# Performance work log

Measured on AMD Instinct MI355X. Metric: run time of the kernel, lower is better.

## Reference

```python
import jax, jax.numpy as jnp
import numpy as np

WS = 7       # window size
SHIFT = 3    # shift size (ws//2)
NH = 16      # num heads
DIM = 512    # channels
HH = 112
WW = 112
HIDDEN = int(DIM * 4.0)
EPS = 1e-5


def _rel_index():
    # Swin relative position index, [N, N] ints into the bias table
    coords = np.stack(np.meshgrid(np.arange(WS), np.arange(WS), indexing='ij')).reshape(2, -1)
    rel = coords[:, :, None] - coords[:, None, :]
    rel = rel.transpose(1, 2, 0) + (WS - 1)
    rel[:, :, 0] *= 2 * WS - 1
    return rel.sum(-1)


def _attn_mask():
    # shifted-window mask on HH x WW (already multiples of WS) -> [nW, N, N] with 0 / -1e9
    img = np.zeros((HH, WW), np.int32)
    cnt = 0
    sl = (slice(0, -WS), slice(-WS, -SHIFT), slice(-SHIFT, None))
    for h in sl:
        for w in sl:
            img[h, w] = cnt
            cnt += 1
    win = img.reshape(HH // WS, WS, WW // WS, WS).transpose(0, 2, 1, 3).reshape(-1, WS * WS)
    diff = win[:, None, :] - win[:, :, None]
    return np.where(diff == 0, 0.0, -1e9).astype(np.float32)


def setup_inputs() -> dict:
    key = jax.random.key(0)
    ks = jax.random.split(key, 8)
    s = 0.02
    return {
        'x': jax.random.normal(ks[0], (DIM, HH, WW), jnp.float32),
        'norm1_w': jnp.ones((DIM,), jnp.float32),
        'norm1_b': jnp.zeros((DIM,), jnp.float32),
        'qkv_w': jax.random.normal(ks[1], (3 * DIM, DIM), jnp.float32) * s,
        'qkv_b': jnp.zeros((3 * DIM,), jnp.float32),
        'proj_w': jax.random.normal(ks[2], (DIM, DIM), jnp.float32) * s,
        'proj_b': jnp.zeros((DIM,), jnp.float32),
        'rpb_table': jax.random.normal(ks[3], ((2 * WS - 1) ** 2, NH), jnp.float32) * s,
        'norm2_w': jnp.ones((DIM,), jnp.float32),
        'norm2_b': jnp.zeros((DIM,), jnp.float32),
        'fc1_w': jax.random.normal(ks[4], (HIDDEN, DIM), jnp.float32) * s,
        'fc1_b': jnp.zeros((HIDDEN,), jnp.float32),
        'fc2_w': jax.random.normal(ks[5], (DIM, HIDDEN), jnp.float32) * s,
        'fc2_b': jnp.zeros((DIM,), jnp.float32),
    }


def _ln(x_hwc, w, b):
    m = x_hwc.mean(-1, keepdims=True)
    v = x_hwc.var(-1, keepdims=True)
    return (x_hwc - m) / jnp.sqrt(v + EPS) * w + b


def reference(x, norm1_w, norm1_b, qkv_w, qkv_b, proj_w, proj_b, rpb_table,
              norm2_w, norm2_b, fc1_w, fc1_b, fc2_w, fc2_b):
    C, H, W = x.shape
    ws = WS
    N = ws * ws
    hd = C // NH
    scale = 1.0 / np.sqrt(hd).astype(np.float32)

    x_hwc = jnp.moveaxis(x, 0, -1)                       # [H,W,C]
    xn = _ln(x_hwc, norm1_w, norm1_b)
    xs = jnp.roll(xn, (-SHIFT, -SHIFT), (0, 1))          # cyclic shift
    # window partition -> [nW, N, C]
    xw = xs.reshape(H // ws, ws, W // ws, ws, C).transpose(0, 2, 1, 3, 4).reshape(-1, N, C)

    qkv = xw @ qkv_w.T + qkv_b                            # [nW,N,3C]
    q, k, v = jnp.split(qkv, 3, -1)
    heads = lambda t: t.reshape(-1, N, NH, hd).transpose(0, 2, 1, 3)  # [nW,H,N,hd]
    q, k, v = heads(q), heads(k), heads(v)

    attn = jnp.einsum('whnd,whmd->whnm', q * scale, k)    # [nW,H,N,N]
    idx = jnp.asarray(_rel_index().reshape(-1))
    bias = rpb_table[idx].reshape(N, N, NH).transpose(2, 0, 1)  # [H,N,N]
    mask = jnp.asarray(_attn_mask())                       # [nW,N,N]
    attn = attn + bias[None] + mask[:, None]
    attn = jax.nn.softmax(attn, -1)

    out = jnp.einsum('whnm,whmd->whnd', attn, v).transpose(0, 2, 1, 3).reshape(-1, N, C)
    out = out @ proj_w.T + proj_b
    # window unpartition + reverse shift
    out = out.reshape(H // ws, W // ws, ws, ws, C).transpose(0, 2, 1, 3, 4).reshape(H, W, C)
    out = jnp.roll(out, (SHIFT, SHIFT), (0, 1))

    x1 = x_hwc + out                                       # residual (DropPath rate 0)
    x2 = _ln(x1, norm2_w, norm2_b)
    h = jax.nn.gelu(x2.reshape(-1, C) @ fc1_w.T + fc1_b)
    m = (h @ fc2_w.T + fc2_b).reshape(H, W, C)
    y = x1 + m
    return jnp.moveaxis(y, -1, 0)                          # back to [C,H,W]
```

## Files before the change

### kernel.cpp

```cpp
#include <hip/hip_runtime.h>

#define NPIX 12544
#define CDIM 512
#define QKVN 1536
#define HIDDEN 2048

typedef unsigned short u16;
typedef unsigned int u32;

typedef short bf16x8 __attribute__((ext_vector_type(8)));
typedef float f32x4 __attribute__((ext_vector_type(4)));

static __device__ __forceinline__ u16 f2bf(float f) {
  u32 u = __float_as_uint(f);
  return (u16)((u + 0x7fffu + ((u >> 16) & 1u)) >> 16);
}
static __device__ __forceinline__ u32 pack2(float a, float b) {
  return (u32)f2bf(a) | ((u32)f2bf(b) << 16);
}
static __device__ __forceinline__ u32 packtrunc2(float lo, float hi) {
  return __builtin_amdgcn_perm(__float_as_uint(hi), __float_as_uint(lo), 0x07060302u);
}
static __device__ __forceinline__ void async_ld16(const void* g, void* l) {
  __builtin_amdgcn_global_load_lds((__attribute__((address_space(1))) void*)g,
                                   (__attribute__((address_space(3))) void*)l, 16, 0, 0);
}

__global__ __launch_bounds__(256) void f32_to_bf16(const float* __restrict__ in, u16* __restrict__ out) {
  const int i = blockIdx.x * 256 + threadIdx.x;
  const float4 v = ((const float4*)in)[i];
  ushort4 u;
  u.x = f2bf(v.x); u.y = f2bf(v.y); u.z = f2bf(v.z); u.w = f2bf(v.w);
  ((ushort4*)out)[i] = u;
}

__global__ __launch_bounds__(256) void ln1_partial(const float* __restrict__ x,
                                                   float* __restrict__ psum, float* __restrict__ pssq) {
  const int p = blockIdx.x * 256 + threadIdx.x;
  const int c0 = blockIdx.y * 32;
  float s = 0.f, ss = 0.f;
#pragma unroll
  for (int c = 0; c < 32; c++) {
    const float v = x[(long)(c0 + c) * NPIX + p];
    s += v; ss += v * v;
  }
  psum[blockIdx.y * NPIX + p] = s;
  pssq[blockIdx.y * NPIX + p] = ss;
}

__global__ __launch_bounds__(256) void ln1_stats(const float* __restrict__ psum, const float* __restrict__ pssq,
                                                 float* __restrict__ mean, float* __restrict__ rstd) {
  const int p = blockIdx.x * 256 + threadIdx.x;
  float s = 0.f, ss = 0.f;
#pragma unroll
  for (int ch = 0; ch < 16; ch++) { s += psum[ch * NPIX + p]; ss += pssq[ch * NPIX + p]; }
  const float m = s * (1.f / 512.f);
  const float v = ss * (1.f / 512.f) - m * m;
  mean[p] = m;
  rstd[p] = rsqrtf(v + 1e-5f);
}

__global__ __launch_bounds__(256) void ln1_shift_part(const float* __restrict__ x,
    const float* __restrict__ mean, const float* __restrict__ rstd,
    const float* __restrict__ gw, const float* __restrict__ gb, u16* __restrict__ xw) {
  __shared__ float tile[32][65];
  const int p0 = blockIdx.x * 64;
  const int c0 = blockIdx.y * 32;
  const int t = threadIdx.x;
  {
    const int pl = t & 63;
    const int cl0 = t >> 6;
#pragma unroll
    for (int r = 0; r < 8; r++) {
      const int cl = r * 4 + cl0;
      tile[cl][pl] = x[(long)(c0 + cl) * NPIX + p0 + pl];
    }
  }
  __syncthreads();
  const int cl = t & 31;
  const int g = t >> 5;
  const float wc = gw[c0 + cl];
  const float bc = gb[c0 + cl];
#pragma unroll
  for (int pass = 0; pass < 8; pass++) {
    const int pl = pass * 8 + g;
    const int p = p0 + pl;
    const int h = p / 112;
    const int w = p - h * 112;
    int hs = h + 109; if (hs >= 112) hs -= 112;
    int ws2 = w + 109; if (ws2 >= 112) ws2 -= 112;
    const int hq = hs / 7, wq = ws2 / 7;
    const int tok = (hq * 16 + wq) * 49 + (hs - hq * 7) * 7 + (ws2 - wq * 7);
    const float val = (tile[cl][pl] - mean[p]) * rstd[p] * wc + bc;
    xw[(long)tok * 512 + c0 + cl] = f2bf(val);
  }
}

template<bool OUT_BF16, bool DO_GELU, bool REMAP>
__global__ __launch_bounds__(256, 2) void gemm_bt(
    const u16* __restrict__ A, const u16* __restrict__ B,
    const float* __restrict__ bias, void* __restrict__ out,
    const int N, const int K) {
  __shared__ __align__(16) u16 Asm[128 * 32];
  __shared__ __align__(16) u16 Bsm[128 * 32];
  const int M0 = blockIdx.x << 7;
  const int N0 = blockIdx.y << 7;
  const int t = threadIdx.x;
  const int wave = t >> 6;
  const int lane = t & 63;
  const int l15 = lane & 15;
  const int quad = lane >> 4;
  const int wm = wave & 1;
  const int wn = wave >> 1;

  f32x4 acc[4][4] = {};

  for (int k0 = 0; k0 < K; k0 += 32) {
#pragma unroll
    for (int i = 0; i < 2; i++) {
      const int flatbase = i * 256 + wave * 64;
      const int FL = flatbase + lane;
      const int row = FL >> 2;
      const int chunk = FL & 3;
      async_ld16(A + (long)(M0 + row) * K + k0 + chunk * 8, &Asm[flatbase * 8]);
      async_ld16(B + (long)(N0 + row) * K + k0 + chunk * 8, &Bsm[flatbase * 8]);
    }
    __syncthreads();
    bf16x8 af[4], bfr[4];
#pragma unroll
    for (int im = 0; im < 4; im++)
      af[im] = *(const bf16x8*)&Asm[(wm * 64 + im * 16 + l15) * 32 + quad * 8];
#pragma unroll
    for (int in = 0; in < 4; in++)
      bfr[in] = *(const bf16x8*)&Bsm[(wn * 64 + in * 16 + l15) * 32 + quad * 8];
#pragma unroll
    for (int im = 0; im < 4; im++)
#pragma unroll
      for (int in = 0; in < 4; in++)
        acc[im][in] = __builtin_amdgcn_mfma_f32_16x16x32_bf16(af[im], bfr[in], acc[im][in], 0, 0, 0);
    __syncthreads();
  }

#pragma unroll
  for (int im = 0; im < 4; im++) {
#pragma unroll
    for (int in = 0; in < 4; in++) {
      const int col = N0 + wn * 64 + in * 16 + l15;
      const float bv = bias[col];
#pragma unroll
      for (int r = 0; r < 4; r++) {
        const int row = M0 + wm * 64 + im * 16 + quad * 4 + r;
        float v = acc[im][in][r] + bv;
        if (DO_GELU) {
          const float z2 = 1.5957691216f * (v + 0.044715f * v * v * v);
          v = v / (1.0f + __expf(-z2));
        }
        long orow = row;
        if (REMAP) {
          const int win = row / 49;
          const int nn = row - win * 49;
          const int nq = nn / 7;
          const int hs = (win >> 4) * 7 + nq;
          const int wsx = (win & 15) * 7 + (nn - nq * 7);
          int h = hs + 3; if (h >= 112) h -= 112;
          int w = wsx + 3; if (w >= 112) w -= 112;
          orow = h * 112 + w;
        }
        if (OUT_BF16) ((u16*)out)[orow * (long)N + col] = f2bf(v);
        else          ((float*)out)[orow * (long)N + col] = v;
      }
    }
  }
}

__global__ __launch_bounds__(256) void build_biasT(const float* __restrict__ rpb, float* __restrict__ biasT) {
  const int cls = blockIdx.x >> 4;
  const int head = blockIdx.x & 15;
  for (int e = threadIdx.x; e < 4096; e += 256) {
    const int j = e >> 6;
    const int i = e & 63;
    float v;
    if (j >= 49) v = -1e9f;
    else if (i >= 49) v = 0.f;
    else {
      const int ri = i / 7, ci = i - (i / 7) * 7;
      const int rj = j / 7, cj = j - (j / 7) * 7;
      v = rpb[((ri - rj + 6) * 13 + (ci - cj + 6)) * 16 + head];
      const int lhi = (cls & 2) ? (ri < 4 ? 1 : 2) : 0;
      const int lwi = (cls & 1) ? (ci < 4 ? 1 : 2) : 0;
      const int lhj = (cls & 2) ? (rj < 4 ? 1 : 2) : 0;
      const int lwj = (cls & 1) ? (cj < 4 ? 1 : 2) : 0;
      if (lhi * 3 + lwi != lhj * 3 + lwj) v = -1e9f;
    }
    biasT[(long)blockIdx.x * 4096 + e] = v;
  }
}

__global__ __launch_bounds__(256, 3) void attn_mfma(
    const u16* __restrict__ qkv, const float* __restrict__ biasT, u16* __restrict__ out) {
  __shared__ __align__(16) u16 slds[24576];
  const int t = threadIdx.x;
  const int wave = t >> 6;
  const int lane = t & 63;
  const int l15 = lane & 15;
  const int quad = lane >> 4;
  const int win = blockIdx.x >> 2;
  const int head = (blockIdx.x & 3) * 4 + wave;
  const int cls = (((win >> 4) == 15) ? 2 : 0) | (((win & 15) == 15) ? 1 : 0);

  u16* Qb  = slds + wave * 6144;
  u16* Kb  = Qb + 2048;
  u16* Vtb = Qb + 4096;
  u16* Pb  = Qb;

  const int rrow = lane >> 2;
  const int chunk = lane & 3;
  uint4 vv[4];
#pragma unroll
  for (int it = 0; it < 4; it++) {
    const int row = it * 16 + rrow;
    const int jc = row < 49 ? row : 48;
    const long gbase = (long)(win * 49 + jc) * 1536 + head * 32 + chunk * 8;
    async_ld16(qkv + gbase,       Qb + it * 512 + lane * 8);
    async_ld16(qkv + gbase + 512, Kb + it * 512 + lane * 8);
    vv[it] = *(const uint4*)(qkv + gbase + 1024);
  }
  __syncthreads();

#pragma unroll
  for (int it = 0; it < 4; it++) {
    const int row = it * 16 + rrow;
    const u32* w = (const u32*)&vv[it];
#pragma unroll
    for (int tt = 0; tt < 8; tt++) {
      const int d = chunk * 8 + tt;
      const u16 val = (tt & 1) ? (u16)(w[tt >> 1] >> 16) : (u16)(w[tt >> 1] & 0xffffu);
      Vtb[d * 64 + (row ^ (((d >> 2) & 3) << 4))] = val;
    }
  }

  bf16x8 kfrag[4], qfrag[4];
#pragma unroll
  for (int jm = 0; jm < 4; jm++)
    kfrag[jm] = *(const bf16x8*)(Kb + (jm * 16 + l15) * 32 + quad * 8);
#pragma unroll
  for (int in = 0; in < 4; in++)
    qfrag[in] = *(const bf16x8*)(Qb + (in * 16 + l15) * 32 + quad * 8);
  f32x4 sacc[4][4] = {};
#pragma unroll
  for (int jm = 0; jm < 4; jm++)
#pragma unroll
    for (int in = 0; in < 4; in++)
      sacc[jm][in] = __builtin_amdgcn_mfma_f32_16x16x32_bf16(kfrag[jm], qfrag[in], sacc[jm][in], 0, 0, 0);

  const float* bT = biasT + (long)(cls * 16 + head) * 4096;
  const float sc = 0.17677669529663687f;
#pragma unroll
  for (int jm = 0; jm < 4; jm++) {
    const float* bp = bT + (jm * 16 + quad * 4) * 64 + l15;
#pragma unroll
    for (int in = 0; in < 4; in++)
#pragma unroll
      for (int r = 0; r < 4; r++)
        sacc[jm][in][r] = sacc[jm][in][r] * sc + bp[r * 64 + in * 16];
  }
  float linv[4];
#pragma unroll
  for (int in = 0; in < 4; in++) {
    float m = -1e30f;
#pragma unroll
    for (int jm = 0; jm < 4; jm++)
#pragma unroll
      for (int r = 0; r < 4; r++) m = fmaxf(m, sacc[jm][in][r]);
    m = fmaxf(m, __shfl_xor(m, 16));
    m = fmaxf(m, __shfl_xor(m, 32));
    float s = 0.f;
#pragma unroll
    for (int jm = 0; jm < 4; jm++)
#pragma unroll
      for (int r = 0; r < 4; r++) {
        const float e = __expf(sacc[jm][in][r] - m);
        sacc[jm][in][r] = e; s += e;
      }
    s += __shfl_xor(s, 16);
    s += __shfl_xor(s, 32);
    linv[in] = __builtin_amdgcn_rcpf(s);
  }

#pragma unroll
  for (int in = 0; in < 4; in++) {
    const int i = in * 16 + l15;
    const int rot = (l15 & 3) << 4;
#pragma unroll
    for (int jm = 0; jm < 4; jm++) {
      const u32 lo = packtrunc2(sacc[jm][in][0], sacc[jm][in][1]);
      const u32 hi = packtrunc2(sacc[jm][in][2], sacc[jm][in][3]);
      uint2 u; u.x = lo; u.y = hi;
      *(uint2*)(Pb + i * 64 + ((jm * 16 + quad * 4) ^ rot)) = u;
    }
  }

  f32x4 oacc[2][4] = {};
#pragma unroll
  for (int ks = 0; ks < 2; ks++) {
    bf16x8 vtf[2], pf[4];
#pragma unroll
    for (int dm = 0; dm < 2; dm++)
      vtf[dm] = *(const bf16x8*)(Vtb + (dm * 16 + l15) * 64 + ((ks * 32 + quad * 8) ^ ((l15 >> 2) << 4)));
#pragma unroll
    for (int in = 0; in < 4; in++)
      pf[in] = *(const bf16x8*)(Pb + (in * 16 + l15) * 64 + ((ks * 32 + quad * 8) ^ ((l15 & 3) << 4)));
#pragma unroll
    for (int dm = 0; dm < 2; dm++)
#pragma unroll
      for (int in = 0; in < 4; in++)
        oacc[dm][in] = __builtin_amdgcn_mfma_f32_16x16x32_bf16(vtf[dm], pf[in], oacc[dm][in], 0, 0, 0);
  }

#pragma unroll
  for (int in = 0; in < 4; in++) {
    const int i = in * 16 + l15;
    if (i < 49) {
      const float inv = linv[in];
      const long base = (long)(win * 49 + i) * 512 + head * 32 + quad * 4;
#pragma unroll
      for (int dm = 0; dm < 2; dm++) {
        const float v0 = oacc[dm][in][0] * inv, v1 = oacc[dm][in][1] * inv;
        const float v2 = oacc[dm][in][2] * inv, v3 = oacc[dm][in][3] * inv;
        uint2 u; u.x = packtrunc2(v0, v1); u.y = packtrunc2(v2, v3);
        *(uint2*)(out + base + dm * 16) = u;
      }
    }
  }
}

__global__ __launch_bounds__(256) void resid_kernel(const float* __restrict__ x,
    const float* __restrict__ proj, float* __restrict__ x1) {
  __shared__ float tile[32][65];
  const int p0 = blockIdx.x * 64;
  const int c0 = blockIdx.y * 32;
  const int t = threadIdx.x;
  {
    const int pl = t & 63;
    const int cl0 = t >> 6;
#pragma unroll
    for (int r = 0; r < 8; r++) {
      const int cl = r * 4 + cl0;
      tile[cl][pl] = x[(long)(c0 + cl) * NPIX + p0 + pl];
    }
  }
  __syncthreads();
  const int cl = t & 31;
  const int g = t >> 5;
#pragma unroll
  for (int pass = 0; pass < 8; pass++) {
    const int pl = pass * 8 + g;
    const long idx = (long)(p0 + pl) * 512 + c0 + cl;
    x1[idx] = tile[cl][pl] + proj[idx];
  }
}

__global__ __launch_bounds__(256) void ln2_apply(const float* __restrict__ x1,
    const float* __restrict__ gw, const float* __restrict__ gb, u16* __restrict__ x2) {
  const int wave = threadIdx.x >> 6;
  const int lane = threadIdx.x & 63;
  const int p = blockIdx.x * 4 + wave;
  const float4* row = (const float4*)(x1 + (long)p * 512);
  const float4 a = row[lane * 2];
  const float4 b = row[lane * 2 + 1];
  float s = a.x + a.y + a.z + a.w + b.x + b.y + b.z + b.w;
  float ss = a.x * a.x + a.y * a.y + a.z * a.z + a.w * a.w
           + b.x * b.x + b.y * b.y + b.z * b.z + b.w * b.w;
#pragma unroll
  for (int o = 32; o > 0; o >>= 1) { s += __shfl_xor(s, o); ss += __shfl_xor(ss, o); }
  const float m = s * (1.f / 512.f);
  const float var = ss * (1.f / 512.f) - m * m;
  const float rs = rsqrtf(var + 1e-5f);
  const float4 w0 = ((const float4*)gw)[lane * 2];
  const float4 w1 = ((const float4*)gw)[lane * 2 + 1];
  const float4 b0 = ((const float4*)gb)[lane * 2];
  const float4 b1 = ((const float4*)gb)[lane * 2 + 1];
  uint4 u;
  u.x = pack2((a.x - m) * rs * w0.x + b0.x, (a.y - m) * rs * w0.y + b0.y);
  u.y = pack2((a.z - m) * rs * w0.z + b0.z, (a.w - m) * rs * w0.w + b0.w);
  u.z = pack2((b.x - m) * rs * w1.x + b1.x, (b.y - m) * rs * w1.y + b1.y);
  u.w = pack2((b.z - m) * rs * w1.z + b1.z, (b.w - m) * rs * w1.w + b1.w);
  ((uint4*)(x2 + (long)p * 512))[lane] = u;
}

__global__ __launch_bounds__(256) void final_kernel(const float* __restrict__ x1,
    const float* __restrict__ mm, float* __restrict__ y) {
  __shared__ float tile[32][65];
  const int p0 = blockIdx.x * 64;
  const int c0 = blockIdx.y * 32;
  const int t = threadIdx.x;
  {
    const int cl = t & 31;
    const int g = t >> 5;
#pragma unroll
    for (int pass = 0; pass < 8; pass++) {
      const int pl = pass * 8 + g;
      const long idx = (long)(p0 + pl) * 512 + c0 + cl;
      tile[cl][pl] = x1[idx] + mm[idx];
    }
  }
  __syncthreads();
  const int pl = t & 63;
  const int cl0 = t >> 6;
#pragma unroll
  for (int r = 0; r < 8; r++) {
    const int cl = r * 4 + cl0;
    y[(long)(c0 + cl) * NPIX + p0 + pl] = tile[cl][pl];
  }
}

extern "C" void kernel_launch(void* const* d_in, const int* in_sizes, int n_in,
                              void* d_out, int out_size, void* d_ws, size_t ws_size,
                              hipStream_t stream) {
  (void)in_sizes; (void)n_in; (void)out_size; (void)ws_size;
  const float* x      = (const float*)d_in[0];
  const float* n1w    = (const float*)d_in[1];
  const float* n1b    = (const float*)d_in[2];
  const float* qkv_w  = (const float*)d_in[3];
  const float* qkv_b  = (const float*)d_in[4];
  const float* proj_w = (const float*)d_in[5];
  const float* proj_b = (const float*)d_in[6];
  const float* rpb    = (const float*)d_in[7];
  const float* n2w    = (const float*)d_in[8];
  const float* n2b    = (const float*)d_in[9];
  const float* fc1_w  = (const float*)d_in[10];
  const float* fc1_b  = (const float*)d_in[11];
  const float* fc2_w  = (const float*)d_in[12];
  const float* fc2_b  = (const float*)d_in[13];
  float* y = (float*)d_out;

  char* base = (char*)d_ws;
  size_t off = 0;
  auto alloc = [&](size_t b) { char* p = base + off; off += (b + 255) & ~(size_t)255; return p; };
  float* mean1 = (float*)alloc((size_t)NPIX * 4);
  float* rstd1 = (float*)alloc((size_t)NPIX * 4);
  float* psum  = (float*)alloc((size_t)16 * NPIX * 4);
  float* pssq  = (float*)alloc((size_t)16 * NPIX * 4);
  u16* Wq = (u16*)alloc((size_t)QKVN * CDIM * 2);
  u16* Wp = (u16*)alloc((size_t)CDIM * CDIM * 2);
  u16* W1 = (u16*)alloc((size_t)HIDDEN * CDIM * 2);
  u16* W2 = (u16*)alloc((size_t)CDIM * HIDDEN * 2);
  float* biasT = (float*)alloc((size_t)4 * 16 * 4096 * 4);
  u16* bufA = (u16*)alloc((size_t)NPIX * CDIM * 2);
  char* bufB = alloc((size_t)NPIX * QKVN * 2);
  float* x1 = (float*)alloc((size_t)NPIX * CDIM * 4);
  u16* hbuf = (u16*)alloc((size_t)NPIX * HIDDEN * 2);

  u16* xw      = bufA;
  u16* qkvbuf  = (u16*)bufB;
  u16* attnout = bufA;
  float* projout = (float*)bufB;
  u16* x2 = bufA;
  float* mbuf = (float*)bufB;

  f32_to_bf16<<<QKVN * CDIM / 1024, 256, 0, stream>>>(qkv_w, Wq);
  f32_to_bf16<<<CDIM * CDIM / 1024, 256, 0, stream>>>(proj_w, Wp);
  f32_to_bf16<<<HIDDEN * CDIM / 1024, 256, 0, stream>>>(fc1_w, W1);
  f32_to_bf16<<<CDIM * HIDDEN / 1024, 256, 0, stream>>>(fc2_w, W2);
  build_biasT<<<64, 256, 0, stream>>>(rpb, biasT);

  ln1_partial<<<dim3(49, 16), 256, 0, stream>>>(x, psum, pssq);
  ln1_stats<<<49, 256, 0, stream>>>(psum, pssq, mean1, rstd1);
  ln1_shift_part<<<dim3(196, 16), 256, 0, stream>>>(x, mean1, rstd1, n1w, n1b, xw);

  gemm_bt<true, false, false><<<dim3(98, QKVN / 128), 256, 0, stream>>>(xw, Wq, qkv_b, qkvbuf, QKVN, CDIM);
  attn_mfma<<<1024, 256, 0, stream>>>(qkvbuf, biasT, attnout);
  gemm_bt<false, false, true><<<dim3(98, CDIM / 128), 256, 0, stream>>>(attnout, Wp, proj_b, projout, CDIM, CDIM);

  resid_kernel<<<dim3(196, 16), 256, 0, stream>>>(x, projout, x1);
  ln2_apply<<<NPIX / 4, 256, 0, stream>>>(x1, n2w, n2b, x2);

  gemm_bt<true, true, false><<<dim3(98, HIDDEN / 128), 256, 0, stream>>>(x2, W1, fc1_b, hbuf, HIDDEN, CDIM);
  gemm_bt<false, false, false><<<dim3(98, CDIM / 128), 256, 0, stream>>>(hbuf, W2, fc2_b, mbuf, CDIM, HIDDEN);

  final_kernel<<<dim3(196, 16), 256, 0, stream>>>(x1, mbuf, y);
}
```

Baseline: 329.2 us.

## Swizzle GEMM/attention LDS tiles, vectorize GEMM epilogue, fuse weight conversions

XOR-swizzles the 16-byte chunk placement in the GEMM and attention LDS tiles so fragment reads avoid bank conflicts. It also swaps the MFMA operand order so each lane holds four consecutive columns, which lets the GEMM epilogue write vectors and load bias as a float4. The four weight-conversion launches are merged into one kernel, and the GEMM occupancy hint rises from 2 to 3 blocks per CU, which may limit registers and cause spills.

After: 331.5 us. About the same (+0.7%).

```diff
diff --git a/kernel.cpp b/kernel.cpp
--- a/kernel.cpp
+++ b/kernel.cpp
@@ -26,12 +26,21 @@
                                    (__attribute__((address_space(3))) void*)l, 16, 0, 0);
 }
 
-__global__ __launch_bounds__(256) void f32_to_bf16(const float* __restrict__ in, u16* __restrict__ out) {
-  const int i = blockIdx.x * 256 + threadIdx.x;
-  const float4 v = ((const float4*)in)[i];
+__global__ __launch_bounds__(256) void convert_weights(
+    const float* __restrict__ qw, const float* __restrict__ pw,
+    const float* __restrict__ w1, const float* __restrict__ w2,
+    u16* __restrict__ Wq, u16* __restrict__ Wp, u16* __restrict__ W1o, u16* __restrict__ W2o) {
+  const int b = blockIdx.x;
+  const float* src; u16* dst; long off;
+  if (b < 768)       { src = qw; dst = Wq;  off = (long)b * 1024; }
+  else if (b < 1024) { src = pw; dst = Wp;  off = (long)(b - 768) * 1024; }
+  else if (b < 2048) { src = w1; dst = W1o; off = (long)(b - 1024) * 1024; }
+  else               { src = w2; dst = W2o; off = (long)(b - 2048) * 1024; }
+  const long i = off / 4 + threadIdx.x;
+  const float4 v = ((const float4*)src)[i];
   ushort4 u;
   u.x = f2bf(v.x); u.y = f2bf(v.y); u.z = f2bf(v.z); u.w = f2bf(v.w);
-  ((ushort4*)out)[i] = u;
+  ((ushort4*)dst)[i] = u;
 }
 
 __global__ __launch_bounds__(256) void ln1_partial(const float* __restrict__ x,
@@ -97,7 +106,7 @@
 }
 
 template<bool OUT_BF16, bool DO_GELU, bool REMAP>
-__global__ __launch_bounds__(256, 2) void gemm_bt(
+__global__ __launch_bounds__(256, 3) void gemm_bt(
     const u16* __restrict__ A, const u16* __restrict__ B,
     const float* __restrict__ bias, void* __restrict__ out,
     const int N, const int K) {
@@ -112,6 +121,7 @@
   const int quad = lane >> 4;
   const int wm = wave & 1;
   const int wn = wave >> 1;
+  const int swz = (l15 >> 1) & 3;
 
   f32x4 acc[4][4] = {};
 
@@ -121,7 +131,7 @@
       const int flatbase = i * 256 + wave * 64;
       const int FL = flatbase + lane;
       const int row = FL >> 2;
-      const int chunk = FL & 3;
+      const int chunk = (FL & 3) ^ ((row >> 1) & 3);
       async_ld16(A + (long)(M0 + row) * K + k0 + chunk * 8, &Asm[flatbase * 8]);
       async_ld16(B + (long)(N0 + row) * K + k0 + chunk * 8, &Bsm[flatbase * 8]);
     }
@@ -129,45 +139,54 @@
     bf16x8 af[4], bfr[4];
 #pragma unroll
     for (int im = 0; im < 4; im++)
-      af[im] = *(const bf16x8*)&Asm[(wm * 64 + im * 16 + l15) * 32 + quad * 8];
+      af[im] = *(const bf16x8*)&Asm[(wm * 64 + im * 16 + l15) * 32 + (quad ^ swz) * 8];
 #pragma unroll
     for (int in = 0; in < 4; in++)
-      bfr[in] = *(const bf16x8*)&Bsm[(wn * 64 + in * 16 + l15) * 32 + quad * 8];
+      bfr[in] = *(const bf16x8*)&Bsm[(wn * 64 + in * 16 + l15) * 32 + (quad ^ swz) * 8];
 #pragma unroll
     for (int im = 0; im < 4; im++)
 #pragma unroll
       for (int in = 0; in < 4; in++)
-        acc[im][in] = __builtin_amdgcn_mfma_f32_16x16x32_bf16(af[im], bfr[in], acc[im][in], 0, 0, 0);
+        acc[im][in] = __builtin_amdgcn_mfma_f32_16x16x32_bf16(bfr[in], af[im], acc[im][in], 0, 0, 0);
     __syncthreads();
   }
 
 #pragma unroll
   for (int im = 0; im < 4; im++) {
+    const int row = M0 + wm * 64 + im * 16 + l15;
+    long orow = row;
+    if (REMAP) {
+      const int win = row / 49;
+      const int nn = row - win * 49;
+      const int nq = nn / 7;
+      const int hs = (win >> 4) * 7 + nq;
+      const int wsx = (win & 15) * 7 + (nn - nq * 7);
+      int h = hs + 3; if (h >= 112) h -= 112;
+      int w = wsx + 3; if (w >= 112) w -= 112;
+      orow = h * 112 + w;
+    }
 #pragma unroll
     for (int in = 0; in < 4; in++) {
-      const int col = N0 + wn * 64 + in * 16 + l15;
-      const float bv = bias[col];
+      const int col0 = N0 + wn * 64 + in * 16 + quad * 4;
+      const float4 bv = *(const float4*)(bias + col0);
+      float v[4];
 #pragma unroll
       for (int r = 0; r < 4; r++) {
-        const int row = M0 + wm * 64 + im * 16 + quad * 4 + r;
-        float v = acc[im][in][r] + bv;
+        float vv = acc[im][in][r] + ((const float*)&bv)[r];
         if (DO_GELU) {
-          const float z2 = 1.5957691216f * (v + 0.044715f * v * v * v);
-          v = v / (1.0f + __expf(-z2));
+          const float z2 = 1.5957691216f * (vv + 0.044715f * vv * vv * vv);
+          vv = vv / (1.0f + __expf(-z2));
         }
-        long orow = row;
-        if (REMAP) {
-          const int win = row / 49;
-          const int nn = row - win * 49;
-          const int nq = nn / 7;
-          const int hs = (win >> 4) * 7 + nq;
-          const int wsx = (win & 15) * 7 + (nn - nq * 7);
-          int h = hs + 3; if (h >= 112) h -= 112;
-          int w = wsx + 3; if (w >= 112) w -= 112;
-          orow = h * 112 + w;
-        }
-        if (OUT_BF16) ((u16*)out)[orow * (long)N + col] = f2bf(v);
-        else          ((float*)out)[orow * (long)N + col] = v;
+        v[r] = vv;
+      }
+      if (OUT_BF16) {
+        uint2 u;
+        u.x = pack2(v[0], v[1]);
+        u.y = pack2(v[2], v[3]);
+        *(uint2*)((u16*)out + orow * (long)N + col0) = u;
+      } else {
+        float4 f; f.x = v[0]; f.y = v[1]; f.z = v[2]; f.w = v[3];
+        *(float4*)((float*)out + orow * (long)N + col0) = f;
       }
     }
   }
@@ -214,7 +233,7 @@
   u16* Pb  = Qb;
 
   const int rrow = lane >> 2;
-  const int chunk = lane & 3;
+  const int chunk = (lane & 3) ^ ((lane >> 3) & 3);
   uint4 vv[4];
 #pragma unroll
   for (int it = 0; it < 4; it++) {
@@ -239,13 +258,14 @@
     }
   }
 
+  const int fswz = (l15 >> 1) & 3;
   bf16x8 kfrag[4], qfrag[4];
 #pragma unroll
   for (int jm = 0; jm < 4; jm++)
-    kfrag[jm] = *(const bf16x8*)(Kb + (jm * 16 + l15) * 32 + quad * 8);
+    kfrag[jm] = *(const bf16x8*)(Kb + (jm * 16 + l15) * 32 + (quad ^ fswz) * 8);
 #pragma unroll
   for (int in = 0; in < 4; in++)
-    qfrag[in] = *(const bf16x8*)(Qb + (in * 16 + l15) * 32 + quad * 8);
+    qfrag[in] = *(const bf16x8*)(Qb + (in * 16 + l15) * 32 + (quad ^ fswz) * 8);
   f32x4 sacc[4][4] = {};
 #pragma unroll
   for (int jm = 0; jm < 4; jm++)
@@ -458,10 +478,7 @@
   u16* x2 = bufA;
   float* mbuf = (float*)bufB;
 
-  f32_to_bf16<<<QKVN * CDIM / 1024, 256, 0, stream>>>(qkv_w, Wq);
-  f32_to_bf16<<<CDIM * CDIM / 1024, 256, 0, stream>>>(proj_w, Wp);
-  f32_to_bf16<<<HIDDEN * CDIM / 1024, 256, 0, stream>>>(fc1_w, W1);
-  f32_to_bf16<<<CDIM * HIDDEN / 1024, 256, 0, stream>>>(fc2_w, W2);
+  convert_weights<<<3072, 256, 0, stream>>>(qkv_w, proj_w, fc1_w, fc2_w, Wq, Wp, W1, W2);
   build_biasT<<<64, 256, 0, stream>>>(rpb, biasT);
 
   ln1_partial<<<dim3(49, 16), 256, 0, stream>>>(x, psum, pssq);
```
